# Performance work log

Hardware: AMD Instinct MI355X
Metric: run time of the kernel (lower is better)

## Reference

```python
import jax, jax.numpy as jnp
import numpy as np

DIM = 1024
B, S = 8, 2048
LN_EPS = 1e-5


def setup_inputs() -> dict:
    key = jax.random.key(0)
    k1, k2, k3 = jax.random.split(key, 3)
    x = jax.random.normal(k1, (B, S, DIM), dtype=jnp.float32)
    # xavier_normal for Linear(dim, 3*dim): std = sqrt(2/(fan_in+fan_out))
    w_qkv = jax.random.normal(k2, (3 * DIM, DIM), dtype=jnp.float32) * np.sqrt(2.0 / (DIM + 3 * DIM))
    w_fc = jax.random.normal(k3, (DIM, DIM), dtype=jnp.float32) * np.sqrt(2.0 / (DIM + DIM))
    b_fc = jnp.zeros((DIM,), dtype=jnp.float32)
    gamma = jnp.ones((DIM,), dtype=jnp.float32)
    beta = jnp.zeros((DIM,), dtype=jnp.float32)
    return {"x": x, "w_qkv": w_qkv, "w_fc": w_fc, "b_fc": b_fc, "gamma": gamma, "beta": beta}


def reference(x, w_qkv, w_fc, b_fc, gamma, beta):
    scaling = DIM ** (-0.5)
    # qkv projection (torch Linear: y = x @ W.T), then chunk into q, k, v
    qkv = jnp.einsum('bsd,ed->bse', x, w_qkv)  # [B, S, 3D]
    q, k, v = jnp.split(qkv, 3, axis=-1)
    # attention scores + softmax over keys
    att = jax.nn.softmax(jnp.einsum('bqd,bkd->bqk', q, k) * scaling, axis=-1)
    # NOTE: faithful to the source einsum 'bqk,bvd->bqd' where k and v are
    # independent summed indices (NOT a standard AV contraction).
    y = jnp.einsum('bqk,bvd->bqd', att, v)
    # fc (dropout is identity in eval mode)
    y = jnp.einsum('bqd,ed->bqe', y, w_fc) + b_fc
    # residual + LayerNorm over last dim
    h = x + y
    mu = jnp.mean(h, axis=-1, keepdims=True)
    var = jnp.var(h, axis=-1, keepdims=True)
    return (h - mu) * jax.lax.rsqrt(var + LN_EPS) * gamma + beta
```

## Files before the change

kernel.cpp:

```cpp
#include <hip/hip_runtime.h>

#define DIM   1024
#define BATCH 8
#define SEQ   2048
#define SCHUNKS 16
#define ROWS_PER_CHUNK (SEQ / SCHUNKS)
#define LN_EPS 1e-5f

__global__ __launch_bounds__(256) void k_partial_colsum(
    const float* __restrict__ x, float* __restrict__ partial) {
  int e = blockIdx.x * 256 + threadIdx.x;
  int b = blockIdx.y;
  int c = blockIdx.z;
  const float* base = x + ((size_t)b * SEQ + (size_t)c * ROWS_PER_CHUNK) * DIM + e;
  float acc = 0.f;
#pragma unroll 8
  for (int s = 0; s < ROWS_PER_CHUNK; ++s) acc += base[(size_t)s * DIM];
  partial[((size_t)c * BATCH + b) * DIM + e] = acc;
}

__global__ __launch_bounds__(256) void k_finish_colsum(
    const float* __restrict__ partial, float* __restrict__ xsum) {
  int i = blockIdx.x * 256 + threadIdx.x;
  float acc = 0.f;
#pragma unroll
  for (int c = 0; c < SCHUNKS; ++c) acc += partial[(size_t)c * BATCH * DIM + i];
  xsum[i] = acc;
}

__global__ __launch_bounds__(256) void k_gemv(
    const float* __restrict__ vin, const float* __restrict__ W,
    const float* __restrict__ bias, float* __restrict__ vout) {
  int wave = threadIdx.x >> 6;
  int lane = threadIdx.x & 63;
  int o = blockIdx.x * 4 + wave;
  int b = o >> 10;
  int d = o & (DIM - 1);
  const float* in = vin + (size_t)b * DIM;
  const float* w  = W + (size_t)d * DIM;
  float acc = 0.f;
#pragma unroll 4
  for (int e = lane; e < DIM; e += 64) acc += in[e] * w[e];
#pragma unroll
  for (int off = 32; off; off >>= 1) acc += __shfl_xor(acc, off, 64);
  if (lane == 0) {
    float r = acc;
    if (bias) r += bias[d];
    vout[o] = r;
  }
}

__global__ __launch_bounds__(256) void k_residual_ln(
    const float* __restrict__ x, const float* __restrict__ z,
    const float* __restrict__ gamma, const float* __restrict__ beta,
    float* __restrict__ out) {
  int row = blockIdx.x;
  int b   = row >> 11;
  int t   = threadIdx.x;

  const float4* xr = (const float4*)(x + (size_t)row * DIM);
  const float4* zr = (const float4*)(z + (size_t)b * DIM);
  float4 xv = xr[t];
  float4 zv = zr[t];
  float4 h;
  h.x = xv.x + zv.x; h.y = xv.y + zv.y; h.z = xv.z + zv.z; h.w = xv.w + zv.w;

  float sum = h.x + h.y + h.z + h.w;
  float ss  = h.x * h.x + h.y * h.y + h.z * h.z + h.w * h.w;
#pragma unroll
  for (int off = 32; off; off >>= 1) {
    sum += __shfl_xor(sum, off, 64);
    ss  += __shfl_xor(ss,  off, 64);
  }

  __shared__ float s_sum[4], s_ss[4];
  int wave = t >> 6, lane = t & 63;
  if (lane == 0) { s_sum[wave] = sum; s_ss[wave] = ss; }
  __syncthreads();
  sum = s_sum[0] + s_sum[1] + s_sum[2] + s_sum[3];
  ss  = s_ss[0]  + s_ss[1]  + s_ss[2]  + s_ss[3];

  const float inv = 1.0f / (float)DIM;
  float mu  = sum * inv;
  float var = ss * inv - mu * mu;
  float rs  = rsqrtf(var + LN_EPS);

  float4 g  = ((const float4*)gamma)[t];
  float4 be = ((const float4*)beta)[t];
  float4 o;
  o.x = (h.x - mu) * rs * g.x + be.x;
  o.y = (h.y - mu) * rs * g.y + be.y;
  o.z = (h.z - mu) * rs * g.z + be.z;
  o.w = (h.w - mu) * rs * g.w + be.w;
  ((float4*)out)[(size_t)row * (DIM / 4) + t] = o;
}

extern "C" void kernel_launch(void* const* d_in, const int* in_sizes, int n_in,
                              void* d_out, int out_size, void* d_ws, size_t ws_size,
                              hipStream_t stream) {
  const float* x     = (const float*)d_in[0];
  const float* w_qkv = (const float*)d_in[1];
  const float* w_fc  = (const float*)d_in[2];
  const float* b_fc  = (const float*)d_in[3];
  const float* gamma = (const float*)d_in[4];
  const float* beta  = (const float*)d_in[5];
  float* out = (float*)d_out;

  float* ws      = (float*)d_ws;
  float* partial = ws;
  float* xsum    = partial + (size_t)SCHUNKS * BATCH * DIM;
  float* vsum    = xsum + (size_t)BATCH * DIM;
  float* z       = vsum + (size_t)BATCH * DIM;

  const float* w_v = w_qkv + (size_t)2 * DIM * DIM;

  dim3 g1(DIM / 256, BATCH, SCHUNKS);
  hipLaunchKernelGGL(k_partial_colsum, g1, dim3(256), 0, stream, x, partial);
  hipLaunchKernelGGL(k_finish_colsum, dim3(BATCH * DIM / 256), dim3(256), 0,
                     stream, partial, xsum);

  hipLaunchKernelGGL(k_gemv, dim3(BATCH * DIM / 4), dim3(256), 0, stream,
                     xsum, w_v, (const float*)nullptr, vsum);
  hipLaunchKernelGGL(k_gemv, dim3(BATCH * DIM / 4), dim3(256), 0, stream,
                     vsum, w_fc, b_fc, z);

  hipLaunchKernelGGL(k_residual_ln, dim3(BATCH * SEQ), dim3(256), 0, stream,
                     x, z, gamma, beta, out);
}
```

Before: 46.11 us.

## Vectorize colsum, gemv and layernorm; one wave per LN row with nontemporal stores

The column-sum kernels now use float4 vector loads, with more sequence chunks (64) so the grid stays large. The gemv loads weights and inputs as float4. Residual+LayerNorm assigns one wavefront per row, which removes the shared-memory reduction and the block barrier, and writes output with nontemporal stores to avoid polluting the cache. The main intent is to cut memory-instruction count and synchronization in the bandwidth-bound passes over x. The price is more per-thread register use and a larger partial-sum workspace.

After: 48.39 us. 4.9% more time.

```diff
diff --git a/kernel.cpp b/kernel.cpp
--- a/kernel.cpp
+++ b/kernel.cpp
@@ -3,29 +3,33 @@
 #define DIM   1024
 #define BATCH 8
 #define SEQ   2048
-#define SCHUNKS 16
-#define ROWS_PER_CHUNK (SEQ / SCHUNKS)
+#define CHUNKS 64
+#define ROWS  (SEQ / CHUNKS)
 #define LN_EPS 1e-5f
+
+typedef float v4 __attribute__((ext_vector_type(4)));
 
 __global__ __launch_bounds__(256) void k_partial_colsum(
     const float* __restrict__ x, float* __restrict__ partial) {
-  int e = blockIdx.x * 256 + threadIdx.x;
+  int c = blockIdx.x;
   int b = blockIdx.y;
-  int c = blockIdx.z;
-  const float* base = x + ((size_t)b * SEQ + (size_t)c * ROWS_PER_CHUNK) * DIM + e;
-  float acc = 0.f;
+  int t = threadIdx.x;
+  const v4* base =
+      (const v4*)(x + ((size_t)b * SEQ + (size_t)c * ROWS) * DIM) + t;
+  v4 acc = {0.f, 0.f, 0.f, 0.f};
 #pragma unroll 8
-  for (int s = 0; s < ROWS_PER_CHUNK; ++s) acc += base[(size_t)s * DIM];
-  partial[((size_t)c * BATCH + b) * DIM + e] = acc;
+  for (int s = 0; s < ROWS; ++s) acc += base[(size_t)s * (DIM / 4)];
+  ((v4*)partial)[((size_t)c * BATCH + b) * (DIM / 4) + t] = acc;
 }
 
 __global__ __launch_bounds__(256) void k_finish_colsum(
     const float* __restrict__ partial, float* __restrict__ xsum) {
-  int i = blockIdx.x * 256 + threadIdx.x;
-  float acc = 0.f;
-#pragma unroll
-  for (int c = 0; c < SCHUNKS; ++c) acc += partial[(size_t)c * BATCH * DIM + i];
-  xsum[i] = acc;
+  int i4 = blockIdx.x * 256 + threadIdx.x;
+  const v4* p = (const v4*)partial;
+  v4 acc = {0.f, 0.f, 0.f, 0.f};
+#pragma unroll 8
+  for (int c = 0; c < CHUNKS; ++c) acc += p[(size_t)c * BATCH * (DIM / 4) + i4];
+  ((v4*)xsum)[i4] = acc;
 }
 
 __global__ __launch_bounds__(256) void k_gemv(
@@ -36,11 +40,15 @@
   int o = blockIdx.x * 4 + wave;
   int b = o >> 10;
   int d = o & (DIM - 1);
-  const float* in = vin + (size_t)b * DIM;
-  const float* w  = W + (size_t)d * DIM;
+  const v4* in4 = (const v4*)(vin + (size_t)b * DIM);
+  const v4* w4  = (const v4*)(W + (size_t)d * DIM);
   float acc = 0.f;
-#pragma unroll 4
-  for (int e = lane; e < DIM; e += 64) acc += in[e] * w[e];
+#pragma unroll
+  for (int j = 0; j < 4; ++j) {
+    v4 w = w4[lane + 64 * j];
+    v4 i = in4[lane + 64 * j];
+    acc += w.x * i.x + w.y * i.y + w.z * i.z + w.w * i.w;
+  }
 #pragma unroll
   for (int off = 32; off; off >>= 1) acc += __shfl_xor(acc, off, 64);
   if (lane == 0) {
@@ -54,45 +62,43 @@
     const float* __restrict__ x, const float* __restrict__ z,
     const float* __restrict__ gamma, const float* __restrict__ beta,
     float* __restrict__ out) {
-  int row = blockIdx.x;
+  int wave = threadIdx.x >> 6;
+  int lane = threadIdx.x & 63;
+  int row = blockIdx.x * 4 + wave;
   int b   = row >> 11;
-  int t   = threadIdx.x;
 
-  const float4* xr = (const float4*)(x + (size_t)row * DIM);
-  const float4* zr = (const float4*)(z + (size_t)b * DIM);
-  float4 xv = xr[t];
-  float4 zv = zr[t];
-  float4 h;
-  h.x = xv.x + zv.x; h.y = xv.y + zv.y; h.z = xv.z + zv.z; h.w = xv.w + zv.w;
+  const v4* xr = (const v4*)(x + (size_t)row * DIM);
+  const v4* zr = (const v4*)(z + (size_t)b * DIM);
 
-  float sum = h.x + h.y + h.z + h.w;
-  float ss  = h.x * h.x + h.y * h.y + h.z * h.z + h.w * h.w;
+  v4 h[4];
+  float sum = 0.f, ss = 0.f;
+#pragma unroll
+  for (int j = 0; j < 4; ++j) {
+    v4 xv = xr[lane + 64 * j];
+    v4 zv = zr[lane + 64 * j];
+    v4 hv = xv + zv;
+    h[j] = hv;
+    sum += hv.x + hv.y + hv.z + hv.w;
+    ss  += hv.x * hv.x + hv.y * hv.y + hv.z * hv.z + hv.w * hv.w;
+  }
 #pragma unroll
   for (int off = 32; off; off >>= 1) {
     sum += __shfl_xor(sum, off, 64);
     ss  += __shfl_xor(ss,  off, 64);
   }
 
-  __shared__ float s_sum[4], s_ss[4];
-  int wave = t >> 6, lane = t & 63;
-  if (lane == 0) { s_sum[wave] = sum; s_ss[wave] = ss; }
-  __syncthreads();
-  sum = s_sum[0] + s_sum[1] + s_sum[2] + s_sum[3];
-  ss  = s_ss[0]  + s_ss[1]  + s_ss[2]  + s_ss[3];
+  const float inv = 1.0f / (float)DIM;
+  float mu = sum * inv;
+  float rs = rsqrtf(ss * inv - mu * mu + LN_EPS);
 
-  const float inv = 1.0f / (float)DIM;
-  float mu  = sum * inv;
-  float var = ss * inv - mu * mu;
-  float rs  = rsqrtf(var + LN_EPS);
-
-  float4 g  = ((const float4*)gamma)[t];
-  float4 be = ((const float4*)beta)[t];
-  float4 o;
-  o.x = (h.x - mu) * rs * g.x + be.x;
-  o.y = (h.y - mu) * rs * g.y + be.y;
-  o.z = (h.z - mu) * rs * g.z + be.z;
-  o.w = (h.w - mu) * rs * g.w + be.w;
-  ((float4*)out)[(size_t)row * (DIM / 4) + t] = o;
+  v4* outr = (v4*)out + (size_t)row * (DIM / 4);
+#pragma unroll
+  for (int j = 0; j < 4; ++j) {
+    v4 g  = ((const v4*)gamma)[lane + 64 * j];
+    v4 be = ((const v4*)beta)[lane + 64 * j];
+    v4 o = (h[j] - mu) * rs * g + be;
+    __builtin_nontemporal_store(o, &outr[lane + 64 * j]);
+  }
 }
 
 extern "C" void kernel_launch(void* const* d_in, const int* in_sizes, int n_in,
@@ -108,22 +114,22 @@
 
   float* ws      = (float*)d_ws;
   float* partial = ws;
-  float* xsum    = partial + (size_t)SCHUNKS * BATCH * DIM;
+  float* xsum    = partial + (size_t)CHUNKS * BATCH * DIM;
   float* vsum    = xsum + (size_t)BATCH * DIM;
   float* z       = vsum + (size_t)BATCH * DIM;
 
   const float* w_v = w_qkv + (size_t)2 * DIM * DIM;
 
-  dim3 g1(DIM / 256, BATCH, SCHUNKS);
-  hipLaunchKernelGGL(k_partial_colsum, g1, dim3(256), 0, stream, x, partial);
-  hipLaunchKernelGGL(k_finish_colsum, dim3(BATCH * DIM / 256), dim3(256), 0,
-                     stream, partial, xsum);
+  hipLaunchKernelGGL(k_partial_colsum, dim3(CHUNKS, BATCH), dim3(256), 0,
+                     stream, x, partial);
+  hipLaunchKernelGGL(k_finish_colsum, dim3(BATCH * DIM / 4 / 256), dim3(256),
+                     0, stream, partial, xsum);
 
   hipLaunchKernelGGL(k_gemv, dim3(BATCH * DIM / 4), dim3(256), 0, stream,
                      xsum, w_v, (const float*)nullptr, vsum);
   hipLaunchKernelGGL(k_gemv, dim3(BATCH * DIM / 4), dim3(256), 0, stream,
                      vsum, w_fc, b_fc, z);
 
-  hipLaunchKernelGGL(k_residual_ln, dim3(BATCH * SEQ), dim3(256), 0, stream,
-                     x, z, gamma, beta, out);
+  hipLaunchKernelGGL(k_residual_ln, dim3(BATCH * SEQ / 4), dim3(256), 0,
+                     stream, x, z, gamma, beta, out);
 }
```
